# Kernel optimization log

Hardware: AMD Instinct MI355X
Metric: run time of the kernel (lower is better)

The kernel has to match this reference:

```python
import jax, jax.numpy as jnp
import numpy as np
from jax import lax

B = 8192      # batch (many parallel RL envs)
E = 16        # token_embed_size
IE = 128      # image_embed_size == semi_memory_size == LSTM hidden
H = 128       # text GRU hidden (text_embedding_size)
W_EMB = 32    # word_embedding_size
T = 20        # text length
V = 100       # text vocab (obs_space['text'])
NACT = 7      # action_space.n
EMB = IE + H  # embedding_size = 256


def setup_inputs() -> dict:
    key = jax.random.key(0)
    ks = jax.random.split(key, 32)
    f = lambda k, shape, s=0.1: (jax.random.normal(k, shape, jnp.float32) * s)
    C1 = IE // 2
    return {
        'image': jax.random.randint(ks[0], (B, 7, 7, 3), 0, 2),
        'memory': jax.random.normal(ks[1], (B, 2 * IE), jnp.float32),
        'text': jax.random.randint(ks[2], (B, T), 0, V),
        'obj_emb': f(ks[3], (11, E)),
        'col_emb': f(ks[4], (6, E)),
        'st_emb': f(ks[5], (2, E)),
        'conv1_w': f(ks[6], (C1, 3 * E, 2, 2)), 'conv1_b': jnp.zeros((C1,), jnp.float32),
        'conv2_w': f(ks[7], (C1, C1, 2, 2)), 'conv2_b': jnp.zeros((C1,), jnp.float32),
        'conv3_w': f(ks[8], (IE, C1, 2, 2)), 'conv3_b': jnp.zeros((IE,), jnp.float32),
        'lstm_wih': f(ks[9], (4 * IE, IE)), 'lstm_whh': f(ks[10], (4 * IE, IE)),
        'lstm_bih': jnp.zeros((4 * IE,), jnp.float32), 'lstm_bhh': jnp.zeros((4 * IE,), jnp.float32),
        'word_emb': f(ks[11], (V, W_EMB)),
        'gru_wih': f(ks[12], (3 * H, W_EMB)), 'gru_whh': f(ks[13], (3 * H, H)),
        'gru_bih': jnp.zeros((3 * H,), jnp.float32), 'gru_bhh': jnp.zeros((3 * H,), jnp.float32),
        'actor_w1': f(ks[14], (EMB, EMB)), 'actor_b1': jnp.zeros((EMB,), jnp.float32),
        'actor_w2': f(ks[15], (NACT, EMB)), 'actor_b2': jnp.zeros((NACT,), jnp.float32),
        'critic_w1': f(ks[16], (EMB, EMB)), 'critic_b1': jnp.zeros((EMB,), jnp.float32),
        'critic_w2': f(ks[17], (1, EMB)), 'critic_b2': jnp.zeros((1,), jnp.float32),
    }


def reference(image, memory, text, obj_emb, col_emb, st_emb,
              conv1_w, conv1_b, conv2_w, conv2_b, conv3_w, conv3_b,
              lstm_wih, lstm_whh, lstm_bih, lstm_bhh,
              word_emb, gru_wih, gru_whh, gru_bih, gru_bhh,
              actor_w1, actor_b1, actor_w2, actor_b2,
              critic_w1, critic_b1, critic_w2, critic_b2):
    Hs = lstm_whh.shape[1]
    # embed + concat (color, object, state) on last dim, then NHWC->NCHW
    im = jnp.concatenate([col_emb[image[..., 1]], obj_emb[image[..., 0]], st_emb[image[..., 2]]], axis=3)
    x = jnp.transpose(im, (0, 3, 1, 2))  # [B, 3E, 7, 7]
    dn = ('NCHW', 'OIHW', 'NCHW')
    conv = lambda x, w, b: lax.conv_general_dilated(x, w, (1, 1), 'VALID', dimension_numbers=dn) + b[None, :, None, None]
    x = jax.nn.relu(conv(x, conv1_w, conv1_b))                                 # [B, 64, 6, 6]
    x = lax.reduce_window(x, -jnp.inf, lax.max, (1, 1, 2, 2), (1, 1, 2, 2), 'VALID')  # [B, 64, 3, 3]
    x = jax.nn.relu(conv(x, conv2_w, conv2_b))                                 # [B, 64, 2, 2]
    x = jax.nn.relu(conv(x, conv3_w, conv3_b))                                 # [B, 128, 1, 1]
    x = x.reshape(x.shape[0], -1)
    # LSTMCell (torch gate order i, f, g, o)
    h, c = memory[:, :Hs], memory[:, Hs:]
    gates = x @ lstm_wih.T + lstm_bih + h @ lstm_whh.T + lstm_bhh
    i, f, g, o = jnp.split(gates, 4, axis=1)
    c = jax.nn.sigmoid(f) * c + jax.nn.sigmoid(i) * jnp.tanh(g)
    h = jax.nn.sigmoid(o) * jnp.tanh(c)
    memory_out = jnp.concatenate([h, c], axis=1)
    # text GRU (torch gate order r, z, n); precompute input-side gates
    wemb = word_emb[text]  # [B, T, 32]
    gi_all = jnp.einsum('btd,gd->btg', wemb, gru_wih) + gru_bih  # [B, T, 3H]
    HH = gru_whh.shape[1]
    def step(ht, gi):
        gh = ht @ gru_whh.T + gru_bhh
        r = jax.nn.sigmoid(gi[:, :HH] + gh[:, :HH])
        z = jax.nn.sigmoid(gi[:, HH:2 * HH] + gh[:, HH:2 * HH])
        n = jnp.tanh(gi[:, 2 * HH:] + r * gh[:, 2 * HH:])
        return (1.0 - z) * n + z * ht, None
    h0 = jnp.zeros((wemb.shape[0], HH), wemb.dtype)
    ht, _ = lax.scan(step, h0, jnp.swapaxes(gi_all, 0, 1))
    emb = jnp.concatenate([h, ht], axis=1)  # [B, 256]
    logits = jnp.tanh(emb @ actor_w1.T + actor_b1) @ actor_w2.T + actor_b2
    log_probs = jax.nn.log_softmax(logits, axis=1)  # Categorical logits
    value = (jnp.tanh(emb @ critic_w1.T + critic_b1) @ critic_w2.T + critic_b2)[:, 0]
    return (log_probs, value, memory_out)
```

## Files before the change

kernel.cpp:

```cpp
#include <hip/hip_runtime.h>

#define Bsz   8192
#define Tlen  20
#define OUT_VAL_OFF  57344
#define OUT_MEM_OFF  65536

#define WS_GI     0
#define WS_D1     153600
#define WS_W2BH   161792
#define WS_W2BL   194560
#define WS_W3BH   227328
#define WS_W3BL   292864
#define WS_WHF    686080
#define WS_WTBH   882688
#define WS_WTBL   1144832
#define WS_LB     1406976
#define WS_C2W    1409024
#define WS_C2B    1474560
#define WS_C3W    1474816
#define WS_C3B    1605888
#define WS_C1B    1606400
#define WS_BH     1606656
#define WS_B1     1608192
#define WS_W2     1610240
#define WS_B2     1618432
#define WS_FLAG   1618464
#define WS_WHB    1618496
#define WS_LWTB   1716800

#define GBLK   512
#define GROWS  16
#define PREP_TASKS 453768

using frag16 = __attribute__((ext_vector_type(8))) short;
using fragf4 = __attribute__((ext_vector_type(4))) float;

__device__ __forceinline__ float bf2f(unsigned short u){
    union { unsigned int i; float f; } v; v.i = ((unsigned int)u) << 16; return v.f;
}
__device__ __forceinline__ unsigned short f2bf(float f){
    union { float f; unsigned int i; } v; v.f = f;
    unsigned int x = v.i;
    return (unsigned short)((x + 0x7fffu + ((x >> 16) & 1u)) >> 16);
}
__device__ __forceinline__ void f2bf2(float f, unsigned short &h, unsigned short &l){
    union { float f; unsigned int i; } u; u.f = f;
    h = (unsigned short)(u.i >> 16);
    union { unsigned int i; float f; } t; t.i = u.i & 0xffff0000u;
    l = f2bf(f - t.f);
}
__device__ __forceinline__ float sigm(float x){ return 1.0f / (1.0f + __expf(-x)); }
__device__ __forceinline__ float tanh_f(float x){ return 1.0f - 2.0f / (__expf(2.0f * x) + 1.0f); }

template<bool BF>
__device__ __forceinline__ float G(const void* p, int i){
    if (BF) return bf2f(((const unsigned short*)p)[i]);
    else    return ((const float*)p)[i];
}

__global__ __launch_bounds__(256) void sniff_kernel(
    const unsigned short* __restrict__ we, int* __restrict__ flag)
{
    __shared__ int cnt;
    if (threadIdx.x == 0) cnt = 0;
    __syncthreads();
    int c = 0;
    for (int i = threadIdx.x; i < 2048; i += 256) {
        int e = (we[i] >> 7) & 0xFF;
        if (e >= 96 && e <= 160) c++;
    }
    atomicAdd(&cnt, c);
    __syncthreads();
    if (threadIdx.x == 0) *flag = (cnt >= 1792) ? 1 : 0;
}

template<bool BF>
__global__ __launch_bounds__(256) void prep_kernel(
    const int* __restrict__ flag,
    const void* word_emb, const void* gru_wih, const void* gru_bih,
    const void* col_emb, const void* obj_emb, const void* st_emb,
    const void* conv1_w, const void* conv1_b,
    const void* conv2_w, const void* conv2_b,
    const void* conv3_w, const void* conv3_b,
    const void* lstm_wih, const void* lstm_whh,
    const void* lstm_bih, const void* lstm_bhh,
    const void* actor_w1, const void* actor_b1,
    const void* actor_w2, const void* actor_b2,
    const void* critic_w1, const void* critic_b1,
    const void* critic_w2, const void* critic_b2,
    const void* gru_whh, const void* gru_bhh,
    float* __restrict__ ws0)
{
    if ((*flag != 0) != BF) return;
    int task = blockIdx.x * 256 + threadIdx.x;
    if (task >= PREP_TASKS) return;
    char* wsb = (char*)ws0;
    if (task < 38400) {
        int v = task / 384, g = task - v * 384;
        float acc = G<BF>(gru_bih, g);
        #pragma unroll
        for (int d = 0; d < 32; d++)
            acc += G<BF>(word_emb, v * 32 + d) * G<BF>(gru_wih, g * 32 + d);
        ((float*)(wsb + WS_GI))[task] = acc;
    } else if (task < 40448) {
        int i2 = task - 38400;
        int o = i2 & 63; int tkk = i2 >> 6;
        int kx = tkk & 1, ky = (tkk >> 1) & 1, t = tkk >> 2;
        int c = t & 1, ob = (t >> 1) & 1, s = (t >> 2) & 1;
        float acc = 0.f;
        #pragma unroll
        for (int i = 0; i < 48; i++) {
            float e;
            if (i < 16)      e = G<BF>(col_emb, c * 16 + i);
            else if (i < 32) e = G<BF>(obj_emb, ob * 16 + (i - 16));
            else             e = G<BF>(st_emb, s * 16 + (i - 32));
            acc += e * G<BF>(conv1_w, ((o * 48 + i) * 2 + ky) * 2 + kx);
        }
        ((float*)(wsb + WS_D1))[tkk * 64 + ((o + tkk) & 63)] = acc;
    } else if (task < 171520) {
        int i3 = task - 40448;
        int u = i3 >> 8, k = i3 & 255;
        float w = (u < 256) ? G<BF>(actor_w1, u * 256 + k)
                            : G<BF>(critic_w1, (u - 256) * 256 + k);
        unsigned short hi = f2bf(w);
        ((unsigned short*)(wsb + WS_WTBH))[i3] = hi;
        ((unsigned short*)(wsb + WS_WTBL))[i3] = f2bf(w - bf2f(hi));
    } else if (task < 172032) {
        int i = task - 171520;
        ((float*)(wsb + WS_LB))[i] = G<BF>(lstm_bih, i) + G<BF>(lstm_bhh, i);
    } else if (task < 188416) {
        int i = task - 172032;
        int o = i & 63, pp = (i >> 6) & 3, ii = i >> 8;
        ((float*)(wsb + WS_C2W))[i] = G<BF>(conv2_w, o * 256 + ii * 4 + pp);
    } else if (task < 188480) {
        int i = task - 188416;
        ((float*)(wsb + WS_C2B))[i] = G<BF>(conv2_b, i);
    } else if (task < 221248) {
        int i = task - 188480;
        int o = i & 127, kk = i >> 7;
        ((float*)(wsb + WS_C3W))[i] = G<BF>(conv3_w, o * 256 + kk);
    } else if (task < 221376) {
        int i = task - 221248;
        ((float*)(wsb + WS_C3B))[i] = G<BF>(conv3_b, i);
    } else if (task < 221440) {
        int i = task - 221376;
        ((float*)(wsb + WS_C1B))[i] = G<BF>(conv1_b, i);
    } else if (task < 221824) {
        int i = task - 221440;
        ((float*)(wsb + WS_BH))[i] = G<BF>(gru_bhh, i);
    } else if (task < 222336) {
        int i = task - 221824;
        ((float*)(wsb + WS_B1))[i] = (i < 256) ? G<BF>(actor_b1, i) : G<BF>(critic_b1, i - 256);
    } else if (task < 224384) {
        int i = task - 222336;
        int u = i >> 8, k = i & 255;
        ((float*)(wsb + WS_W2))[i] = (u < 7) ? G<BF>(actor_w2, u * 256 + k) : G<BF>(critic_w2, k);
    } else if (task < 224392) {
        int i = task - 224384;
        ((float*)(wsb + WS_B2))[i] = (i < 7) ? G<BF>(actor_b2, i) : G<BF>(critic_b2, 0);
    } else if (task < 273544) {
        int i = task - 224392;
        ((unsigned short*)(wsb + WS_WHB))[i] = f2bf(G<BF>(gru_whh, i));
    } else if (task < 404616) {
        int i = task - 273544;
        int g = i >> 8, k = i & 255;
        float v = (k < 128) ? G<BF>(lstm_wih, g * 128 + k)
                            : G<BF>(lstm_whh, g * 128 + (k - 128));
        ((unsigned short*)(wsb + WS_LWTB))[i] = f2bf(v);
    } else if (task < 421000) {
        int i = task - 404616;
        float w = G<BF>(conv2_w, i);
        unsigned short hi = f2bf(w);
        ((unsigned short*)(wsb + WS_W2BH))[i] = hi;
        ((unsigned short*)(wsb + WS_W2BL))[i] = f2bf(w - bf2f(hi));
    } else {
        int i = task - 421000;
        float w = G<BF>(conv3_w, i);
        unsigned short hi = f2bf(w);
        ((unsigned short*)(wsb + WS_W3BH))[i] = hi;
        ((unsigned short*)(wsb + WS_W3BL))[i] = f2bf(w - bf2f(hi));
    }
}

__global__ __launch_bounds__(256) void conv_kernel(
    const int* __restrict__ image,
    const float* __restrict__ ws0,
    float* __restrict__ mem_out)
{
    const char* wsb = (const char*)ws0;
    const float* D1g  = (const float*)(wsb + WS_D1);
    const float* c1bF = (const float*)(wsb + WS_C1B);
    const float* c2bF = (const float*)(wsb + WS_C2B);
    const float* c3bF = (const float*)(wsb + WS_C3B);
    const unsigned short* w2bh = (const unsigned short*)(wsb + WS_W2BH);
    const unsigned short* w2bl = (const unsigned short*)(wsb + WS_W2BL);
    const unsigned short* w3bh = (const unsigned short*)(wsb + WS_W3BH);
    const unsigned short* w3bl = (const unsigned short*)(wsb + WS_W3BL);

    __shared__ __align__(16) unsigned short sp1h[4608];
    __shared__ __align__(16) unsigned short sp1l[4608];
    __shared__ __align__(16) unsigned short sA3h[9 * 264];
    __shared__ __align__(16) unsigned short sA3l[9 * 264];
    __shared__ __align__(16) float sD1[2048];
    __shared__ unsigned char stt[392];

    int tid = threadIdx.x;
    int b0 = blockIdx.x * 8;
    int wave = tid >> 6, lane = tid & 63;
    int quad = lane >> 4, l16 = lane & 15;

    for (int i = tid; i < 2048; i += 256) sD1[i] = D1g[i];
    for (int i = tid; i < 392; i += 256) {
        int s = i / 49, p = i - s * 49;
        int base = ((b0 + s) * 49 + p) * 3;
        stt[i] = (unsigned char)(image[base + 1] | (image[base] << 1) | (image[base + 2] << 2));
    }
    for (int i = tid; i < 264; i += 256) { sA3h[8 * 264 + i] = 0; sA3l[8 * 264 + i] = 0; }
    __syncthreads();

    for (int task = tid; task < 4608; task += 256) {
        int s = task & 7;
        int op = task >> 3;
        int o = op / 9, p = op - o * 9;
        int py = p / 3, px = p - py * 3;
        float bo = c1bF[o];
        float mx = 0.f;
        #pragma unroll
        for (int dy = 0; dy < 2; dy++)
        #pragma unroll
        for (int dx = 0; dx < 2; dx++) {
            int y = 2 * py + dy, x = 2 * px + dx;
            float sum = bo;
            #pragma unroll
            for (int ky = 0; ky < 2; ky++)
            #pragma unroll
            for (int kx = 0; kx < 2; kx++) {
                int t = stt[s * 49 + (y + ky) * 7 + (x + kx)];
                int tkk = t * 4 + ky * 2 + kx;
                sum += sD1[tkk * 64 + ((o + tkk) & 63)];
            }
            mx = fmaxf(mx, sum);
        }
        unsigned short h, l;
        f2bf2(mx, h, l);
        sp1h[op * 8 + s] = h;
        sp1l[op * 8 + s] = l;
    }
    __syncthreads();

    {
        int Mt  = wave >> 1;
        int NtB = (wave & 1) * 2;
        int s_a = Mt * 4 + (l16 >> 2);
        int p2  = l16 & 3;
        int bp  = 3 * (p2 >> 1) + (p2 & 1);
        fragf4 acc0 = {0.f,0.f,0.f,0.f}, acc1 = {0.f,0.f,0.f,0.f};
        int u0 = (NtB * 16 + l16) * 256;
        int u1 = u0 + 16 * 256;
        #pragma unroll
        for (int kc = 0; kc < 8; kc++) {
            int k0 = kc * 32 + quad * 8;
            int i0 = k0 >> 2;
            const unsigned short* hp = sp1h + (i0 * 9 + bp) * 8 + s_a;
            const unsigned short* lp = sp1l + (i0 * 9 + bp) * 8 + s_a;
            frag16 Ah, Al;
            Ah[0] = (short)hp[0];  Ah[1] = (short)hp[8];
            Ah[2] = (short)hp[24]; Ah[3] = (short)hp[32];
            Ah[4] = (short)hp[72]; Ah[5] = (short)hp[80];
            Ah[6] = (short)hp[96]; Ah[7] = (short)hp[104];
            Al[0] = (short)lp[0];  Al[1] = (short)lp[8];
            Al[2] = (short)lp[24]; Al[3] = (short)lp[32];
            Al[4] = (short)lp[72]; Al[5] = (short)lp[80];
            Al[6] = (short)lp[96]; Al[7] = (short)lp[104];
            frag16 W0h = *(const frag16*)(w2bh + u0 + k0);
            frag16 W0l = *(const frag16*)(w2bl + u0 + k0);
            frag16 W1h = *(const frag16*)(w2bh + u1 + k0);
            frag16 W1l = *(const frag16*)(w2bl + u1 + k0);
            acc0 = __builtin_amdgcn_mfma_f32_16x16x32_bf16(Ah, W0h, acc0, 0, 0, 0);
            acc0 = __builtin_amdgcn_mfma_f32_16x16x32_bf16(Al, W0h, acc0, 0, 0, 0);
            acc0 = __builtin_amdgcn_mfma_f32_16x16x32_bf16(Ah, W0l, acc0, 0, 0, 0);
            acc1 = __builtin_amdgcn_mfma_f32_16x16x32_bf16(Ah, W1h, acc1, 0, 0, 0);
            acc1 = __builtin_amdgcn_mfma_f32_16x16x32_bf16(Al, W1h, acc1, 0, 0, 0);
            acc1 = __builtin_amdgcn_mfma_f32_16x16x32_bf16(Ah, W1l, acc1, 0, 0, 0);
        }
        int sC = Mt * 4 + quad;
        #pragma unroll
        for (int nt = 0; nt < 2; nt++) {
            fragf4 a = nt ? acc1 : acc0;
            int o2 = (NtB + nt) * 16 + l16;
            float b = c2bF[o2];
            #pragma unroll
            for (int reg = 0; reg < 4; reg++) {
                float v = fmaxf(a[reg] + b, 0.f);
                unsigned short h, l;
                f2bf2(v, h, l);
                sA3h[sC * 264 + o2 * 4 + reg] = h;
                sA3l[sC * 264 + o2 * 4 + reg] = l;
            }
        }
    }
    __syncthreads();

    {
        int NtB = wave * 2;
        int s_a = (l16 < 8) ? l16 : 8;
        fragf4 acc0 = {0.f,0.f,0.f,0.f}, acc1 = {0.f,0.f,0.f,0.f};
        int u0 = (NtB * 16 + l16) * 256;
        int u1 = u0 + 16 * 256;
        #pragma unroll
        for (int kc = 0; kc < 8; kc++) {
            int k0 = kc * 32 + quad * 8;
            frag16 Ah = *(const frag16*)(sA3h + s_a * 264 + k0);
            frag16 Al = *(const frag16*)(sA3l + s_a * 264 + k0);
            frag16 W0h = *(const frag16*)(w3bh + u0 + k0);
            frag16 W0l = *(const frag16*)(w3bl + u0 + k0);
            frag16 W1h = *(const frag16*)(w3bh + u1 + k0);
            frag16 W1l = *(const frag16*)(w3bl + u1 + k0);
            acc0 = __builtin_amdgcn_mfma_f32_16x16x32_bf16(Ah, W0h, acc0, 0, 0, 0);
            acc0 = __builtin_amdgcn_mfma_f32_16x16x32_bf16(Al, W0h, acc0, 0, 0, 0);
            acc0 = __builtin_amdgcn_mfma_f32_16x16x32_bf16(Ah, W0l, acc0, 0, 0, 0);
            acc1 = __builtin_amdgcn_mfma_f32_16x16x32_bf16(Ah, W1h, acc1, 0, 0, 0);
            acc1 = __builtin_amdgcn_mfma_f32_16x16x32_bf16(Al, W1h, acc1, 0, 0, 0);
            acc1 = __builtin_amdgcn_mfma_f32_16x16x32_bf16(Ah, W1l, acc1, 0, 0, 0);
        }
        if (quad < 2) {
            #pragma unroll
            for (int nt = 0; nt < 2; nt++) {
                fragf4 a = nt ? acc1 : acc0;
                int o3 = (NtB + nt) * 16 + l16;
                float b = c3bF[o3];
                #pragma unroll
                for (int reg = 0; reg < 4; reg++) {
                    int s = quad * 4 + reg;
                    mem_out[(b0 + s) * 256 + o3] = fmaxf(a[reg] + b, 0.f);
                }
            }
        }
    }
}

#define GI_LOAD(dst, t) do {                                                  \
    _Pragma("unroll")                                                         \
    for (int rg_ = 0; rg_ < 4; rg_++) {                                       \
        int tok_ = sTok2[(m0 + rg_) * Tlen + (t)];                            \
        const float* gp_ = gi_table + tok_ * 384 + j;                         \
        dst[rg_ * 3 + 0] = gp_[0];                                            \
        dst[rg_ * 3 + 1] = gp_[128];                                          \
        dst[rg_ * 3 + 2] = gp_[256];                                          \
    }                                                                         \
} while (0)

#define GRU_STEP(SRD, SWR, GC, GN, T) do {                                    \
    frag16 Af_[4];                                                            \
    _Pragma("unroll")                                                         \
    for (int kc_ = 0; kc_ < 4; kc_++)                                         \
        Af_[kc_] = *(const frag16*)((SRD) + l16 * 136 + kc_ * 32 + quad * 8); \
    fragf4 aR_ = {0.f,0.f,0.f,0.f}, aZ_ = {0.f,0.f,0.f,0.f};                  \
    fragf4 aN_ = {0.f,0.f,0.f,0.f};                                           \
    _Pragma("unroll")                                                         \
    for (int kc_ = 0; kc_ < 4; kc_++) {                                       \
        aR_ = __builtin_amdgcn_mfma_f32_16x16x32_bf16(Af_[kc_], Bf0[kc_], aR_, 0, 0, 0); \
        aZ_ = __builtin_amdgcn_mfma_f32_16x16x32_bf16(Af_[kc_], Bf1[kc_], aZ_, 0, 0, 0); \
        aN_ = __builtin_amdgcn_mfma_f32_16x16x32_bf16(Af_[kc_], Bf2[kc_], aN_, 0, 0, 0); \
    }                                                                         \
    if ((T) < Tlen - 1) GI_LOAD(GN, (T) + 1);                                 \
    _Pragma("unroll")                                                         \
    for (int reg_ = 0; reg_ < 4; reg_++) {                                    \
        float rg2_ = sigm(GC[reg_*3+0] + aR_[reg_] + bh0);                    \
        float zg_  = sigm(GC[reg_*3+1] + aZ_[reg_] + bh1);                    \
        float ng_  = tanh_f(GC[reg_*3+2] + rg2_ * (aN_[reg_] + bh2));         \
        float hn_  = (1.f - zg_) * ng_ + zg_ * hpv[reg_];                     \
        unsigned short hb_ = f2bf(hn_);                                       \
        hpv[reg_] = bf2f(hb_);                                                \
        (SWR)[(m0 + reg_) * 136 + j] = hb_;                                   \
    }                                                                         \
    __syncthreads();                                                          \
} while (0)

__global__ __launch_bounds__(512, 4) void gru_head_kernel(
    const int* __restrict__ flag,
    const int* __restrict__ text, const void* memory,
    const float* __restrict__ ws0,
    float* __restrict__ mem_out,
    float* __restrict__ out_lp, float* __restrict__ out_val)
{
    const char* wsb = (const char*)ws0;
    const unsigned short* whb2 = (const unsigned short*)(wsb + WS_WHB);
    const unsigned short* lwtb = (const unsigned short*)(wsb + WS_LWTB);
    const unsigned short* wtbh = (const unsigned short*)(wsb + WS_WTBH);
    const unsigned short* wtbl = (const unsigned short*)(wsb + WS_WTBL);
    const float* gi_table = (const float*)(wsb + WS_GI);
    const float* bhF      = (const float*)(wsb + WS_BH);
    const float* b1F      = (const float*)(wsb + WS_B1);
    const float* W2f      = (const float*)(wsb + WS_W2);
    const float* B2f      = (const float*)(wsb + WS_B2);
    const float* lbF      = (const float*)(wsb + WS_LB);

    __shared__ __align__(16) char sU[25600];
    __shared__ float sScore[64];
    __shared__ int   sTok2[320];

    unsigned short* sEh  = (unsigned short*)sU;
    unsigned short* sEl  = (unsigned short*)(sU + 8448);
    unsigned short* sHtA = (unsigned short*)(sU + 16896);
    unsigned short* sHtB = (unsigned short*)(sU + 21248);
    float* sHid = (float*)sU;

    int tid = threadIdx.x;
    int rbase = blockIdx.x * GROWS;
    int wave = tid >> 6, lane = tid & 63;
    int quad = lane >> 4, l16 = lane & 15;
    int j = wave * 16 + l16;
    int m0 = quad * 4;
    const bool bfin = (*flag != 0);
    const unsigned short* mem16 = (const unsigned short*)memory;
    const float*          memf  = (const float*)memory;

    for (int i = tid; i < 4096; i += 512) {
        int m = i >> 8, k = i & 255;
        float v;
        if (k < 128) v = mem_out[(rbase + m) * 256 + k];
        else v = bfin ? bf2f(mem16[(rbase + m) * 256 + (k - 128)])
                      : memf[(rbase + m) * 256 + (k - 128)];
        sEh[m * 264 + k] = f2bf(v);
    }
    for (int i = tid; i < 2176; i += 512) sHtA[i] = 0;
    if (tid < 320) sTok2[tid] = text[rbase * Tlen + tid];
    __syncthreads();

    {
        frag16 Ax[8];
        #pragma unroll
        for (int kc = 0; kc < 8; kc++)
            Ax[kc] = *(const frag16*)(sEh + l16 * 264 + kc * 32 + quad * 8);
        fragf4 aI = {0.f,0.f,0.f,0.f}, aF = {0.f,0.f,0.f,0.f};
        fragf4 aG = {0.f,0.f,0.f,0.f}, aO = {0.f,0.f,0.f,0.f};
        #pragma unroll
        for (int kc = 0; kc < 8; kc++) {
            int ko = kc * 32 + quad * 8;
            frag16 bI = *(const frag16*)(lwtb + (j)       * 256 + ko);
            frag16 bF = *(const frag16*)(lwtb + (128 + j) * 256 + ko);
            frag16 bG = *(const frag16*)(lwtb + (256 + j) * 256 + ko);
            frag16 bO = *(const frag16*)(lwtb + (384 + j) * 256 + ko);
            aI = __builtin_amdgcn_mfma_f32_16x16x32_bf16(Ax[kc], bI, aI, 0, 0, 0);
            aF = __builtin_amdgcn_mfma_f32_16x16x32_bf16(Ax[kc], bF, aF, 0, 0, 0);
            aG = __builtin_amdgcn_mfma_f32_16x16x32_bf16(Ax[kc], bG, aG, 0, 0, 0);
            aO = __builtin_amdgcn_mfma_f32_16x16x32_bf16(Ax[kc], bO, aO, 0, 0, 0);
        }
        float lbI = lbF[j], lbFg = lbF[128 + j], lbG = lbF[256 + j], lbO = lbF[384 + j];
        __syncthreads();
        #pragma unroll
        for (int reg = 0; reg < 4; reg++) {
            int m = m0 + reg;
            float ig = sigm(aI[reg] + lbI);
            float fg = sigm(aF[reg] + lbFg);
            float gv = tanh_f(aG[reg] + lbG);
            float og = sigm(aO[reg] + lbO);
            float cv = bfin ? bf2f(mem16[(rbase + m) * 256 + 128 + j])
                            : memf[(rbase + m) * 256 + 128 + j];
            float cn = fg * cv + ig * gv;
            float hn = og * tanh_f(cn);
            mem_out[(rbase + m) * 256 + j]       = hn;
            mem_out[(rbase + m) * 256 + 128 + j] = cn;
            unsigned short hh = f2bf(hn);
            sEh[m * 264 + j] = hh;
            sEl[m * 264 + j] = f2bf(hn - bf2f(hh));
        }
    }

    frag16 Bf0[4], Bf1[4], Bf2[4];
    #pragma unroll
    for (int kc = 0; kc < 4; kc++) {
        int ko = kc * 32 + quad * 8;
        Bf0[kc] = *(const frag16*)(whb2 + (j)       * 128 + ko);
        Bf1[kc] = *(const frag16*)(whb2 + (128 + j) * 128 + ko);
        Bf2[kc] = *(const frag16*)(whb2 + (256 + j) * 128 + ko);
    }
    float bh0 = bhF[j], bh1 = bhF[128 + j], bh2 = bhF[256 + j];
    float hpv[4] = { 0.f, 0.f, 0.f, 0.f };
    float ga[12], gb[12];

    GI_LOAD(ga, 0);

    for (int tt = 0; tt < 10; tt++) {
        int t0 = tt * 2;
        GRU_STEP(sHtA, sHtB, ga, gb, t0);
        GRU_STEP(sHtB, sHtA, gb, ga, t0 + 1);
    }

    #pragma unroll
    for (int reg = 0; reg < 4; reg++) {
        int m = m0 + reg;
        sEh[m * 264 + 128 + j] = f2bf(hpv[reg]);
    }
    __syncthreads();

    fragf4 acc[4];
    {
        fragf4 z4 = {0.f,0.f,0.f,0.f};
        #pragma unroll
        for (int jb = 0; jb < 4; jb++) acc[jb] = z4;
        #pragma unroll
        for (int kc = 0; kc < 8; kc++) {
            int ko = kc * 32 + quad * 8;
            frag16 Eh = *(const frag16*)(sEh + l16 * 264 + ko);
            #pragma unroll
            for (int jb = 0; jb < 4; jb++) {
                int u = jb * 128 + wave * 16 + l16;
                frag16 Wh = *(const frag16*)(wtbh + u * 256 + ko);
                frag16 Wl = *(const frag16*)(wtbl + u * 256 + ko);
                acc[jb] = __builtin_amdgcn_mfma_f32_16x16x32_bf16(Eh, Wh, acc[jb], 0, 0, 0);
                acc[jb] = __builtin_amdgcn_mfma_f32_16x16x32_bf16(Eh, Wl, acc[jb], 0, 0, 0);
            }
            if (kc < 4) {
                frag16 El = *(const frag16*)(sEl + l16 * 264 + ko);
                #pragma unroll
                for (int jb = 0; jb < 4; jb++) {
                    int u = jb * 128 + wave * 16 + l16;
                    frag16 Wh = *(const frag16*)(wtbh + u * 256 + ko);
                    acc[jb] = __builtin_amdgcn_mfma_f32_16x16x32_bf16(El, Wh, acc[jb], 0, 0, 0);
                }
            }
        }
    }
    __syncthreads();

    #pragma unroll
    for (int half = 0; half < 2; half++) {
        if ((quad >> 1) == half) {
            #pragma unroll
            for (int jb = 0; jb < 4; jb++) {
                int u = jb * 128 + wave * 16 + l16;
                float bu = b1F[u];
                #pragma unroll
                for (int reg = 0; reg < 4; reg++) {
                    int mm = (m0 & 7) + reg;
                    sHid[u * 8 + ((mm + (u & 7)) & 7)] = tanh_f(acc[jb][reg] + bu);
                }
            }
        }
        __syncthreads();
        float acc2 = 0.f;
        int r = tid >> 3, i = tid & 7;
        if (tid < 64) {
            acc2 = B2f[i];
            const float* wrp = W2f + i * 256;
            int ubase = (i < 7) ? 0 : 256;
            for (int k = 0; k < 256; k++) {
                int u = ubase + k;
                acc2 += wrp[k] * sHid[u * 8 + ((r + (u & 7)) & 7)];
            }
            sScore[tid] = acc2;
        }
        __syncthreads();
        if (tid < 64) {
            const float* sr = sScore + r * 8;
            float mx = sr[0];
            #pragma unroll
            for (int a = 1; a < 7; a++) mx = fmaxf(mx, sr[a]);
            float se = 0.f;
            #pragma unroll
            for (int a = 0; a < 7; a++) se += __expf(sr[a] - mx);
            float lse = mx + __logf(se);
            int row = rbase + half * 8 + r;
            if (i < 7) out_lp[row * 7 + i] = acc2 - lse;
            else       out_val[row] = acc2;
        }
        if (half == 0) __syncthreads();
    }
}

extern "C" void kernel_launch(void* const* d_in, const int* in_sizes, int n_in,
                              void* d_out, int out_size, void* d_ws, size_t ws_size,
                              hipStream_t stream) {
    const int*  image  = (const int*)d_in[0];
    const void* memory = d_in[1];
    const int*  text   = (const int*)d_in[2];

    char* wsb = (char*)d_ws;
    float* ws0  = (float*)wsb;
    int*   flag = (int*)(wsb + WS_FLAG);

    float* out = (float*)d_out;
    float* out_lp  = out;
    float* out_val = out + OUT_VAL_OFF;
    float* mem_out = out + OUT_MEM_OFF;

    sniff_kernel<<<1, 256, 0, stream>>>((const unsigned short*)d_in[16], flag);

    const int PREP_GRID = (PREP_TASKS + 255) / 256;
    prep_kernel<true><<<PREP_GRID, 256, 0, stream>>>(flag,
        d_in[16], d_in[17], d_in[19], d_in[4], d_in[3], d_in[5],
        d_in[6], d_in[7], d_in[8], d_in[9], d_in[10], d_in[11],
        d_in[12], d_in[13], d_in[14], d_in[15],
        d_in[21], d_in[22], d_in[23], d_in[24],
        d_in[25], d_in[26], d_in[27], d_in[28],
        d_in[18], d_in[20], ws0);
    prep_kernel<false><<<PREP_GRID, 256, 0, stream>>>(flag,
        d_in[16], d_in[17], d_in[19], d_in[4], d_in[3], d_in[5],
        d_in[6], d_in[7], d_in[8], d_in[9], d_in[10], d_in[11],
        d_in[12], d_in[13], d_in[14], d_in[15],
        d_in[21], d_in[22], d_in[23], d_in[24],
        d_in[25], d_in[26], d_in[27], d_in[28],
        d_in[18], d_in[20], ws0);

    conv_kernel<<<Bsz / 8, 256, 0, stream>>>(image, ws0, mem_out);

    gru_head_kernel<<<GBLK, 512, 0, stream>>>(flag, text, memory, ws0,
                                              mem_out, out_lp, out_val);
}
```

Measured before the change: 266.9 us.

## Fuse conv stack into GRU/head kernel and parallelize the head reduction

After: 269.7 us. Within noise of the previous version (+1.0%).

```diff
diff --git a/kernel.cpp b/kernel.cpp
--- a/kernel.cpp
+++ b/kernel.cpp
@@ -182,163 +182,6 @@
     }
 }
 
-__global__ __launch_bounds__(256) void conv_kernel(
-    const int* __restrict__ image,
-    const float* __restrict__ ws0,
-    float* __restrict__ mem_out)
-{
-    const char* wsb = (const char*)ws0;
-    const float* D1g  = (const float*)(wsb + WS_D1);
-    const float* c1bF = (const float*)(wsb + WS_C1B);
-    const float* c2bF = (const float*)(wsb + WS_C2B);
-    const float* c3bF = (const float*)(wsb + WS_C3B);
-    const unsigned short* w2bh = (const unsigned short*)(wsb + WS_W2BH);
-    const unsigned short* w2bl = (const unsigned short*)(wsb + WS_W2BL);
-    const unsigned short* w3bh = (const unsigned short*)(wsb + WS_W3BH);
-    const unsigned short* w3bl = (const unsigned short*)(wsb + WS_W3BL);
-
-    __shared__ __align__(16) unsigned short sp1h[4608];
-    __shared__ __align__(16) unsigned short sp1l[4608];
-    __shared__ __align__(16) unsigned short sA3h[9 * 264];
-    __shared__ __align__(16) unsigned short sA3l[9 * 264];
-    __shared__ __align__(16) float sD1[2048];
-    __shared__ unsigned char stt[392];
-
-    int tid = threadIdx.x;
-    int b0 = blockIdx.x * 8;
-    int wave = tid >> 6, lane = tid & 63;
-    int quad = lane >> 4, l16 = lane & 15;
-
-    for (int i = tid; i < 2048; i += 256) sD1[i] = D1g[i];
-    for (int i = tid; i < 392; i += 256) {
-        int s = i / 49, p = i - s * 49;
-        int base = ((b0 + s) * 49 + p) * 3;
-        stt[i] = (unsigned char)(image[base + 1] | (image[base] << 1) | (image[base + 2] << 2));
-    }
-    for (int i = tid; i < 264; i += 256) { sA3h[8 * 264 + i] = 0; sA3l[8 * 264 + i] = 0; }
-    __syncthreads();
-
-    for (int task = tid; task < 4608; task += 256) {
-        int s = task & 7;
-        int op = task >> 3;
-        int o = op / 9, p = op - o * 9;
-        int py = p / 3, px = p - py * 3;
-        float bo = c1bF[o];
-        float mx = 0.f;
-        #pragma unroll
-        for (int dy = 0; dy < 2; dy++)
-        #pragma unroll
-        for (int dx = 0; dx < 2; dx++) {
-            int y = 2 * py + dy, x = 2 * px + dx;
-            float sum = bo;
-            #pragma unroll
-            for (int ky = 0; ky < 2; ky++)
-            #pragma unroll
-            for (int kx = 0; kx < 2; kx++) {
-                int t = stt[s * 49 + (y + ky) * 7 + (x + kx)];
-                int tkk = t * 4 + ky * 2 + kx;
-                sum += sD1[tkk * 64 + ((o + tkk) & 63)];
-            }
-            mx = fmaxf(mx, sum);
-        }
-        unsigned short h, l;
-        f2bf2(mx, h, l);
-        sp1h[op * 8 + s] = h;
-        sp1l[op * 8 + s] = l;
-    }
-    __syncthreads();
-
-    {
-        int Mt  = wave >> 1;
-        int NtB = (wave & 1) * 2;
-        int s_a = Mt * 4 + (l16 >> 2);
-        int p2  = l16 & 3;
-        int bp  = 3 * (p2 >> 1) + (p2 & 1);
-        fragf4 acc0 = {0.f,0.f,0.f,0.f}, acc1 = {0.f,0.f,0.f,0.f};
-        int u0 = (NtB * 16 + l16) * 256;
-        int u1 = u0 + 16 * 256;
-        #pragma unroll
-        for (int kc = 0; kc < 8; kc++) {
-            int k0 = kc * 32 + quad * 8;
-            int i0 = k0 >> 2;
-            const unsigned short* hp = sp1h + (i0 * 9 + bp) * 8 + s_a;
-            const unsigned short* lp = sp1l + (i0 * 9 + bp) * 8 + s_a;
-            frag16 Ah, Al;
-            Ah[0] = (short)hp[0];  Ah[1] = (short)hp[8];
-            Ah[2] = (short)hp[24]; Ah[3] = (short)hp[32];
-            Ah[4] = (short)hp[72]; Ah[5] = (short)hp[80];
-            Ah[6] = (short)hp[96]; Ah[7] = (short)hp[104];
-            Al[0] = (short)lp[0];  Al[1] = (short)lp[8];
-            Al[2] = (short)lp[24]; Al[3] = (short)lp[32];
-            Al[4] = (short)lp[72]; Al[5] = (short)lp[80];
-            Al[6] = (short)lp[96]; Al[7] = (short)lp[104];
-            frag16 W0h = *(const frag16*)(w2bh + u0 + k0);
-            frag16 W0l = *(const frag16*)(w2bl + u0 + k0);
-            frag16 W1h = *(const frag16*)(w2bh + u1 + k0);
-            frag16 W1l = *(const frag16*)(w2bl + u1 + k0);
-            acc0 = __builtin_amdgcn_mfma_f32_16x16x32_bf16(Ah, W0h, acc0, 0, 0, 0);
-            acc0 = __builtin_amdgcn_mfma_f32_16x16x32_bf16(Al, W0h, acc0, 0, 0, 0);
-            acc0 = __builtin_amdgcn_mfma_f32_16x16x32_bf16(Ah, W0l, acc0, 0, 0, 0);
-            acc1 = __builtin_amdgcn_mfma_f32_16x16x32_bf16(Ah, W1h, acc1, 0, 0, 0);
-            acc1 = __builtin_amdgcn_mfma_f32_16x16x32_bf16(Al, W1h, acc1, 0, 0, 0);
-            acc1 = __builtin_amdgcn_mfma_f32_16x16x32_bf16(Ah, W1l, acc1, 0, 0, 0);
-        }
-        int sC = Mt * 4 + quad;
-        #pragma unroll
-        for (int nt = 0; nt < 2; nt++) {
-            fragf4 a = nt ? acc1 : acc0;
-            int o2 = (NtB + nt) * 16 + l16;
-            float b = c2bF[o2];
-            #pragma unroll
-            for (int reg = 0; reg < 4; reg++) {
-                float v = fmaxf(a[reg] + b, 0.f);
-                unsigned short h, l;
-                f2bf2(v, h, l);
-                sA3h[sC * 264 + o2 * 4 + reg] = h;
-                sA3l[sC * 264 + o2 * 4 + reg] = l;
-            }
-        }
-    }
-    __syncthreads();
-
-    {
-        int NtB = wave * 2;
-        int s_a = (l16 < 8) ? l16 : 8;
-        fragf4 acc0 = {0.f,0.f,0.f,0.f}, acc1 = {0.f,0.f,0.f,0.f};
-        int u0 = (NtB * 16 + l16) * 256;
-        int u1 = u0 + 16 * 256;
-        #pragma unroll
-        for (int kc = 0; kc < 8; kc++) {
-            int k0 = kc * 32 + quad * 8;
-            frag16 Ah = *(const frag16*)(sA3h + s_a * 264 + k0);
-            frag16 Al = *(const frag16*)(sA3l + s_a * 264 + k0);
-            frag16 W0h = *(const frag16*)(w3bh + u0 + k0);
-            frag16 W0l = *(const frag16*)(w3bl + u0 + k0);
-            frag16 W1h = *(const frag16*)(w3bh + u1 + k0);
-            frag16 W1l = *(const frag16*)(w3bl + u1 + k0);
-            acc0 = __builtin_amdgcn_mfma_f32_16x16x32_bf16(Ah, W0h, acc0, 0, 0, 0);
-            acc0 = __builtin_amdgcn_mfma_f32_16x16x32_bf16(Al, W0h, acc0, 0, 0, 0);
-            acc0 = __builtin_amdgcn_mfma_f32_16x16x32_bf16(Ah, W0l, acc0, 0, 0, 0);
-            acc1 = __builtin_amdgcn_mfma_f32_16x16x32_bf16(Ah, W1h, acc1, 0, 0, 0);
-            acc1 = __builtin_amdgcn_mfma_f32_16x16x32_bf16(Al, W1h, acc1, 0, 0, 0);
-            acc1 = __builtin_amdgcn_mfma_f32_16x16x32_bf16(Ah, W1l, acc1, 0, 0, 0);
-        }
-        if (quad < 2) {
-            #pragma unroll
-            for (int nt = 0; nt < 2; nt++) {
-                fragf4 a = nt ? acc1 : acc0;
-                int o3 = (NtB + nt) * 16 + l16;
-                float b = c3bF[o3];
-                #pragma unroll
-                for (int reg = 0; reg < 4; reg++) {
-                    int s = quad * 4 + reg;
-                    mem_out[(b0 + s) * 256 + o3] = fmaxf(a[reg] + b, 0.f);
-                }
-            }
-        }
-    }
-}
-
 #define GI_LOAD(dst, t) do {                                                  \
     _Pragma("unroll")                                                         \
     for (int rg_ = 0; rg_ < 4; rg_++) {                                       \
@@ -379,6 +222,7 @@
 
 __global__ __launch_bounds__(512, 4) void gru_head_kernel(
     const int* __restrict__ flag,
+    const int* __restrict__ image,
     const int* __restrict__ text, const void* memory,
     const float* __restrict__ ws0,
     float* __restrict__ mem_out,
@@ -389,6 +233,14 @@
     const unsigned short* lwtb = (const unsigned short*)(wsb + WS_LWTB);
     const unsigned short* wtbh = (const unsigned short*)(wsb + WS_WTBH);
     const unsigned short* wtbl = (const unsigned short*)(wsb + WS_WTBL);
+    const unsigned short* w2bh = (const unsigned short*)(wsb + WS_W2BH);
+    const unsigned short* w2bl = (const unsigned short*)(wsb + WS_W2BL);
+    const unsigned short* w3bh = (const unsigned short*)(wsb + WS_W3BH);
+    const unsigned short* w3bl = (const unsigned short*)(wsb + WS_W3BL);
+    const float* D1g      = (const float*)(wsb + WS_D1);
+    const float* c1bF     = (const float*)(wsb + WS_C1B);
+    const float* c2bF     = (const float*)(wsb + WS_C2B);
+    const float* c3bF     = (const float*)(wsb + WS_C3B);
     const float* gi_table = (const float*)(wsb + WS_GI);
     const float* bhF      = (const float*)(wsb + WS_BH);
     const float* b1F      = (const float*)(wsb + WS_B1);
@@ -396,18 +248,26 @@
     const float* B2f      = (const float*)(wsb + WS_B2);
     const float* lbF      = (const float*)(wsb + WS_LB);
 
-    __shared__ __align__(16) char sU[25600];
-    __shared__ float sScore[64];
+    __shared__ __align__(16) char sU[16896 + 45840];
+    __shared__ float sScore[128];
     __shared__ int   sTok2[320];
 
-    unsigned short* sEh  = (unsigned short*)sU;
-    unsigned short* sEl  = (unsigned short*)(sU + 8448);
-    unsigned short* sHtA = (unsigned short*)(sU + 16896);
-    unsigned short* sHtB = (unsigned short*)(sU + 21248);
-    float* sHid = (float*)sU;
+    unsigned short* sEh = (unsigned short*)sU;
+    unsigned short* sEl = (unsigned short*)(sU + 8448);
+    char* R2 = sU + 16896;
+    unsigned char*  stt  = (unsigned char*)R2;
+    float*          sD1  = (float*)(R2 + 784);
+    unsigned short* sp1h = (unsigned short*)(R2 + 8976);
+    unsigned short* sp1l = (unsigned short*)(R2 + 27408);
+    unsigned short* sA3h = (unsigned short*)(R2 + 8976);
+    unsigned short* sA3l = (unsigned short*)(R2 + 17424);
+    unsigned short* sHtA = (unsigned short*)R2;
+    unsigned short* sHtB = (unsigned short*)(R2 + 4352);
+    float*          sHid = (float*)R2;
 
     int tid = threadIdx.x;
     int rbase = blockIdx.x * GROWS;
+    int b0 = rbase;
     int wave = tid >> 6, lane = tid & 63;
     int quad = lane >> 4, l16 = lane & 15;
     int j = wave * 16 + l16;
@@ -416,16 +276,127 @@
     const unsigned short* mem16 = (const unsigned short*)memory;
     const float*          memf  = (const float*)memory;
 
-    for (int i = tid; i < 4096; i += 512) {
-        int m = i >> 8, k = i & 255;
-        float v;
-        if (k < 128) v = mem_out[(rbase + m) * 256 + k];
-        else v = bfin ? bf2f(mem16[(rbase + m) * 256 + (k - 128)])
-                      : memf[(rbase + m) * 256 + (k - 128)];
-        sEh[m * 264 + k] = f2bf(v);
-    }
-    for (int i = tid; i < 2176; i += 512) sHtA[i] = 0;
     if (tid < 320) sTok2[tid] = text[rbase * Tlen + tid];
+    for (int i = tid; i < 2048; i += 512) {
+        int m = i >> 7, k = i & 127;
+        float v = bfin ? bf2f(mem16[(rbase + m) * 256 + k])
+                       : memf[(rbase + m) * 256 + k];
+        sEh[m * 264 + 128 + k] = f2bf(v);
+    }
+    for (int i = tid; i < 2048; i += 512) sD1[i] = D1g[i];
+    for (int i = tid; i < 784; i += 512) {
+        int s = i / 49, p = i - s * 49;
+        int base = ((b0 + s) * 49 + p) * 3;
+        stt[i] = (unsigned char)(image[base + 1] | (image[base] << 1) | (image[base + 2] << 2));
+    }
+    __syncthreads();
+
+    for (int task = tid; task < 9216; task += 512) {
+        int s = task & 15;
+        int op = task >> 4;
+        int o = op / 9, p = op - o * 9;
+        int py = p / 3, px = p - py * 3;
+        float bo = c1bF[o];
+        float mx = 0.f;
+        #pragma unroll
+        for (int dy = 0; dy < 2; dy++)
+        #pragma unroll
+        for (int dx = 0; dx < 2; dx++) {
+            int y = 2 * py + dy, x = 2 * px + dx;
+            float sum = bo;
+            #pragma unroll
+            for (int ky = 0; ky < 2; ky++)
+            #pragma unroll
+            for (int kx = 0; kx < 2; kx++) {
+                int t = stt[s * 49 + (y + ky) * 7 + (x + kx)];
+                int tkk = t * 4 + ky * 2 + kx;
+                sum += sD1[tkk * 64 + ((o + tkk) & 63)];
+            }
+            mx = fmaxf(mx, sum);
+        }
+        unsigned short h, l;
+        f2bf2(mx, h, l);
+        sp1h[op * 16 + s] = h;
+        sp1l[op * 16 + s] = l;
+    }
+    __syncthreads();
+
+    {
+        int Mt  = wave >> 1;
+        int NtB = (wave & 1) * 2;
+        int s_a = Mt * 4 + (l16 >> 2);
+        int p2  = l16 & 3;
+        int bp  = 3 * (p2 >> 1) + (p2 & 1);
+        fragf4 acc0 = {0.f,0.f,0.f,0.f}, acc1 = {0.f,0.f,0.f,0.f};
+        int u0 = (NtB * 16 + l16) * 256;
+        int u1 = u0 + 16 * 256;
+        #pragma unroll
+        for (int kc = 0; kc < 8; kc++) {
+            int k0 = kc * 32 + quad * 8;
+            int i0 = k0 >> 2;
+            const unsigned short* hp = sp1h + (i0 * 9 + bp) * 16 + s_a;
+            const unsigned short* lp = sp1l + (i0 * 9 + bp) * 16 + s_a;
+            frag16 Ah, Al;
+            Ah[0] = (short)hp[0];   Ah[1] = (short)hp[16];
+            Ah[2] = (short)hp[48];  Ah[3] = (short)hp[64];
+            Ah[4] = (short)hp[144]; Ah[5] = (short)hp[160];
+            Ah[6] = (short)hp[192]; Ah[7] = (short)hp[208];
+            Al[0] = (short)lp[0];   Al[1] = (short)lp[16];
+            Al[2] = (short)lp[48];  Al[3] = (short)lp[64];
+            Al[4] = (short)lp[144]; Al[5] = (short)lp[160];
+            Al[6] = (short)lp[192]; Al[7] = (short)lp[208];
+            frag16 W0h = *(const frag16*)(w2bh + u0 + k0);
+            frag16 W0l = *(const frag16*)(w2bl + u0 + k0);
+            frag16 W1h = *(const frag16*)(w2bh + u1 + k0);
+            frag16 W1l = *(const frag16*)(w2bl + u1 + k0);
+            acc0 = __builtin_amdgcn_mfma_f32_16x16x32_bf16(Ah, W0h, acc0, 0, 0, 0);
+            acc0 = __builtin_amdgcn_mfma_f32_16x16x32_bf16(Al, W0h, acc0, 0, 0, 0);
+            acc0 = __builtin_amdgcn_mfma_f32_16x16x32_bf16(Ah, W0l, acc0, 0, 0, 0);
+            acc1 = __builtin_amdgcn_mfma_f32_16x16x32_bf16(Ah, W1h, acc1, 0, 0, 0);
+            acc1 = __builtin_amdgcn_mfma_f32_16x16x32_bf16(Al, W1h, acc1, 0, 0, 0);
+            acc1 = __builtin_amdgcn_mfma_f32_16x16x32_bf16(Ah, W1l, acc1, 0, 0, 0);
+        }
+        __syncthreads();
+        int sC = Mt * 4 + quad;
+        #pragma unroll
+        for (int nt = 0; nt < 2; nt++) {
+            fragf4 a = nt ? acc1 : acc0;
+            int o2 = (NtB + nt) * 16 + l16;
+            float b = c2bF[o2];
+            #pragma unroll
+            for (int reg = 0; reg < 4; reg++) {
+                float v = fmaxf(a[reg] + b, 0.f);
+                unsigned short h, l;
+                f2bf2(v, h, l);
+                sA3h[sC * 264 + o2 * 4 + reg] = h;
+                sA3l[sC * 264 + o2 * 4 + reg] = l;
+            }
+        }
+    }
+    __syncthreads();
+
+    {
+        fragf4 acc0 = {0.f,0.f,0.f,0.f};
+        int u0 = (wave * 16 + l16) * 256;
+        #pragma unroll
+        for (int kc = 0; kc < 8; kc++) {
+            int k0 = kc * 32 + quad * 8;
+            frag16 Ah = *(const frag16*)(sA3h + l16 * 264 + k0);
+            frag16 Al = *(const frag16*)(sA3l + l16 * 264 + k0);
+            frag16 W0h = *(const frag16*)(w3bh + u0 + k0);
+            frag16 W0l = *(const frag16*)(w3bl + u0 + k0);
+            acc0 = __builtin_amdgcn_mfma_f32_16x16x32_bf16(Ah, W0h, acc0, 0, 0, 0);
+            acc0 = __builtin_amdgcn_mfma_f32_16x16x32_bf16(Al, W0h, acc0, 0, 0, 0);
+            acc0 = __builtin_amdgcn_mfma_f32_16x16x32_bf16(Ah, W0l, acc0, 0, 0, 0);
+        }
+        int o3 = wave * 16 + l16;
+        float b = c3bF[o3];
+        #pragma unroll
+        for (int reg = 0; reg < 4; reg++) {
+            int s = quad * 4 + reg;
+            sEh[s * 264 + o3] = f2bf(fmaxf(acc0[reg] + b, 0.f));
+        }
+    }
     __syncthreads();
 
     {
@@ -467,6 +438,7 @@
             sEl[m * 264 + j] = f2bf(hn - bf2f(hh));
         }
     }
+    for (int i = tid; i < 2176; i += 512) { sHtA[i] = 0; sHtB[i] = 0; }
 
     frag16 Bf0[4], Bf1[4], Bf2[4];
     #pragma unroll
@@ -481,6 +453,7 @@
     float ga[12], gb[12];
 
     GI_LOAD(ga, 0);
+    __syncthreads();
 
     for (int tt = 0; tt < 10; tt++) {
         int t0 = tt * 2;
@@ -526,47 +499,47 @@
     __syncthreads();
 
     #pragma unroll
-    for (int half = 0; half < 2; half++) {
-        if ((quad >> 1) == half) {
-            #pragma unroll
-            for (int jb = 0; jb < 4; jb++) {
-                int u = jb * 128 + wave * 16 + l16;
-                float bu = b1F[u];
-                #pragma unroll
-                for (int reg = 0; reg < 4; reg++) {
-                    int mm = (m0 & 7) + reg;
-                    sHid[u * 8 + ((mm + (u & 7)) & 7)] = tanh_f(acc[jb][reg] + bu);
-                }
-            }
-        }
-        __syncthreads();
-        float acc2 = 0.f;
+    for (int jb = 0; jb < 4; jb++) {
+        int u = jb * 128 + wave * 16 + l16;
+        float bu = b1F[u];
+        #pragma unroll
+        for (int reg = 0; reg < 4; reg++) {
+            int m = m0 + reg;
+            sHid[u * 16 + ((m + l16) & 15)] = tanh_f(acc[jb][reg] + bu);
+        }
+    }
+    __syncthreads();
+
+    {
+        int out = tid >> 2, kq = tid & 3;
+        int r = out >> 3, i = out & 7;
+        const float* wrp = W2f + i * 256;
+        int ubase = (i < 7) ? 0 : 256;
+        float ps = 0.f;
+        int kb = kq * 64;
+        for (int kk = 0; kk < 64; kk++) {
+            int u = ubase + kb + kk;
+            ps += wrp[kb + kk] * sHid[u * 16 + ((r + (u & 15)) & 15)];
+        }
+        ps += __shfl_xor(ps, 1);
+        ps += __shfl_xor(ps, 2);
+        if (kq == 0) sScore[out] = ps + B2f[i];
+    }
+    __syncthreads();
+
+    if (tid < 128) {
         int r = tid >> 3, i = tid & 7;
-        if (tid < 64) {
-            acc2 = B2f[i];
-            const float* wrp = W2f + i * 256;
-            int ubase = (i < 7) ? 0 : 256;
-            for (int k = 0; k < 256; k++) {
-                int u = ubase + k;
-                acc2 += wrp[k] * sHid[u * 8 + ((r + (u & 7)) & 7)];
-            }
-            sScore[tid] = acc2;
-        }
-        __syncthreads();
-        if (tid < 64) {
-            const float* sr = sScore + r * 8;
-            float mx = sr[0];
-            #pragma unroll
-            for (int a = 1; a < 7; a++) mx = fmaxf(mx, sr[a]);
-            float se = 0.f;
-            #pragma unroll
-            for (int a = 0; a < 7; a++) se += __expf(sr[a] - mx);
-            float lse = mx + __logf(se);
-            int row = rbase + half * 8 + r;
-            if (i < 7) out_lp[row * 7 + i] = acc2 - lse;
-            else       out_val[row] = acc2;
-        }
-        if (half == 0) __syncthreads();
+        float sc = sScore[tid];
+        const float* sr = sScore + r * 8;
+        float mx = sr[0];
+        #pragma unroll
+        for (int a = 1; a < 7; a++) mx = fmaxf(mx, sr[a]);
+        float se = 0.f;
+        #pragma unroll
+        for (int a = 0; a < 7; a++) se += __expf(sr[a] - mx);
+        float lse = mx + __logf(se);
+        if (i < 7) out_lp[(rbase + r) * 7 + i] = sc - lse;
+        else       out_val[rbase + r] = sc;
     }
 }
 
@@ -604,8 +577,6 @@
         d_in[25], d_in[26], d_in[27], d_in[28],
         d_in[18], d_in[20], ws0);
 
-    conv_kernel<<<Bsz / 8, 256, 0, stream>>>(image, ws0, mem_out);
-
-    gru_head_kernel<<<GBLK, 512, 0, stream>>>(flag, text, memory, ws0,
+    gru_head_kernel<<<GBLK, 512, 0, stream>>>(flag, image, text, memory, ws0,
                                               mem_out, out_lp, out_val);
 }
```
